# Kernel optimization log

Measured on AMD Instinct MI355X. Metric: run time of the kernel, lower is better.

Reference implementation:

```python
import jax, jax.numpy as jnp
import numpy as np

N = 50000        # n_nodes
E = 800000       # n_edges (avg degree 16)
H = 64           # hidden_size
ALPHA = 0.5      # CRF alpha
BETA = 0.5       # CRF beta
N_LAYER = 2      # args.crf_layer
GAMMA = 0.2      # LeakyReLU negative slope


def setup_inputs() -> dict:
    key = jax.random.key(0)
    k = jax.random.split(key, 5)
    emb = jax.random.normal(k[0], (N, H), jnp.float32)
    W_fc = jax.random.normal(k[1], (H, H), jnp.float32) / np.sqrt(H)
    attn_fc_w = jax.random.normal(k[2], (1, 2 * H), jnp.float32) / np.sqrt(2 * H)
    src = jax.random.randint(k[3], (E,), 0, N, dtype=jnp.int32)
    dst = jax.random.randint(k[4], (E,), 0, N, dtype=jnp.int32)
    return {"emb": emb, "W_fc": W_fc, "attn_fc_w": attn_fc_w, "src": src, "dst": dst}


def _segment_softmax(e, dst, n):
    # softmax over incoming edges of each destination node (DGL mailbox softmax)
    m = jax.ops.segment_max(e, dst, num_segments=n)
    m = jnp.where(jnp.isfinite(m), m, 0.0)  # nodes with no in-edges
    ex = jnp.exp(e - m[dst])
    denom = jax.ops.segment_sum(ex, dst, num_segments=n)
    return ex / jnp.maximum(denom[dst], 1e-16)


def reference(emb, W_fc, attn_fc_w, src, dst):
    # attn_fc(concat(z_src, z_dst)) split into two per-node projections
    a_src = attn_fc_w[0, :H]
    a_dst = attn_fc_w[0, H:]
    h = emb
    e = None
    for _ in range(N_LAYER):
        z = h @ W_fc.T                              # [N, H] emb_attn
        e = (z @ a_src)[src] + (z @ a_dst)[dst]     # [E] edge logits
        e = jnp.where(e > 0, e, GAMMA * e)          # LeakyReLU(gamma)
        att = _segment_softmax(e, dst, N)           # [E]
        crf = jax.ops.segment_sum(att[:, None] * h[src], dst, num_segments=N)  # [N, H]
        h = (ALPHA * emb + BETA * crf) / (ALPHA + BETA)
    # training loss (is_train=True); reuses last layer's edge logits e
    loss_a = jnp.sum((h - emb) ** 2, axis=-1)                     # [N]
    att = _segment_softmax(e, dst, N)
    diff = jnp.sqrt(jnp.sum((h[dst] - h[src]) ** 2, axis=-1) + 1e-12)  # [E] L2 norm
    loss_b = jax.ops.segment_sum(att * diff, dst, num_segments=N)  # [N]
    loss = jnp.mean(ALPHA * loss_a + BETA * loss_b)
    return h, loss
```

## Files before the change

### kernel.cpp

```cpp
#include <hip/hip_runtime.h>

#define NNODES 50000
#define NEDGES 800000
#define HDIM 64
#define CAP 64
#define GAMMA 0.2f
#define SCAN_B 256
#define SCAN_NB ((NNODES + SCAN_B - 1) / SCAN_B)
#define LOSS_GRID 2048
#define NPART 8
#define NODES_PER_PART ((NNODES + NPART - 1) / NPART)
#define FILL_SLICES 192
#define E4 (NEDGES / 4)
#define CHUNK ((E4 + FILL_SLICES - 1) / FILL_SLICES)

typedef unsigned short u16;
typedef unsigned int u32;

__device__ __forceinline__ u16 f2bf(float f) {
    u32 u = __float_as_uint(f);
    u32 r = (u + 0x7FFFu + ((u >> 16) & 1u)) >> 16;
    return (u16)r;
}
__device__ __forceinline__ float bflo(u32 u) { return __uint_as_float(u << 16); }
__device__ __forceinline__ float bfhi(u32 u) { return __uint_as_float(u & 0xFFFF0000u); }

__device__ __forceinline__ float wave_sum(float v) {
    #pragma unroll
    for (int off = 32; off; off >>= 1) v += __shfl_xor(v, off, 64);
    return v;
}
__device__ __forceinline__ float wave_max(float v) {
    #pragma unroll
    for (int off = 32; off; off >>= 1) v = fmaxf(v, __shfl_xor(v, off, 64));
    return v;
}
__device__ __forceinline__ int wave_sum_i(int v) {
    #pragma unroll
    for (int off = 32; off; off >>= 1) v += __shfl_xor(v, off, 64);
    return v;
}
__device__ __forceinline__ float group8_sum(float v) {
    v += __shfl_xor(v, 1, 64);
    v += __shfl_xor(v, 2, 64);
    v += __shfl_xor(v, 4, 64);
    return v;
}

__global__ __launch_bounds__(256) void k_init(int* __restrict__ cursor,
                                              float* __restrict__ lossAcc,
                                              const float* __restrict__ Wfc,
                                              const float* __restrict__ attn,
                                              float* __restrict__ ws, float* __restrict__ wd) {
    int t = threadIdx.x;
    int idx = blockIdx.x * 256 + t;
    if (idx < NNODES) cursor[idx] = 0;
    if (blockIdx.x == gridDim.x - 1) {
        if (t >= 80 && t < 96) lossAcc[t - 80] = 0.f;
        if (t >= 128) {
            int tt = t - 128;
            int k = tt & 63;
            const float* av = attn + ((tt >= 64) ? HDIM : 0);
            float s = 0.f;
            for (int j = 0; j < HDIM; ++j) s += Wfc[j * HDIM + k] * av[j];
            if (tt < 64) ws[k] = s; else wd[k] = s;
        }
    }
}

__global__ __launch_bounds__(256) void k_fillx(const int4* __restrict__ src4,
                                               const int4* __restrict__ dst4,
                                               int* __restrict__ cursor,
                                               u16* __restrict__ padded) {
    const int part = blockIdx.x & (NPART - 1);
    const int slice = blockIdx.x >> 3;
    const int lo = slice * CHUNK;
    const int hi = min(lo + CHUNK, E4);
    const int plo = part * NODES_PER_PART;
    const int phi = plo + NODES_PER_PART;
    for (int i = lo + threadIdx.x; i < hi; i += 256) {
        int4 d = dst4[i];
        bool mx = d.x >= plo && d.x < phi;
        bool my = d.y >= plo && d.y < phi;
        bool mz = d.z >= plo && d.z < phi;
        bool mw = d.w >= plo && d.w < phi;
        if (mx | my | mz | mw) {
            int4 s = src4[i];
            if (mx) { int p0 = atomicAdd(&cursor[d.x], 1); if (p0 < CAP) padded[d.x * CAP + p0] = (u16)s.x; }
            if (my) { int p1 = atomicAdd(&cursor[d.y], 1); if (p1 < CAP) padded[d.y * CAP + p1] = (u16)s.y; }
            if (mz) { int p2 = atomicAdd(&cursor[d.z], 1); if (p2 < CAP) padded[d.z * CAP + p2] = (u16)s.z; }
            if (mw) { int p3 = atomicAdd(&cursor[d.w], 1); if (p3 < CAP) padded[d.w * CAP + p3] = (u16)s.w; }
        }
    }
}

__global__ __launch_bounds__(256) void k_scan1z(const int* __restrict__ deg,
                                                int* __restrict__ blockSums,
                                                const float* __restrict__ emb,
                                                const float* __restrict__ ws,
                                                const float* __restrict__ wd,
                                                u16* __restrict__ emb_bf,
                                                float* __restrict__ zs, float* __restrict__ zd) {
    int t = threadIdx.x;
    if (blockIdx.x < SCAN_NB) {
        int idx = blockIdx.x * SCAN_B + t;
        int v = (idx < NNODES) ? min(deg[idx], CAP) : 0;
        int wsum = wave_sum_i(v);
        __shared__ int part[4];
        if ((t & 63) == 0) part[t >> 6] = wsum;
        __syncthreads();
        if (t == 0) blockSums[blockIdx.x] = part[0] + part[1] + part[2] + part[3];
    }
    int tid = blockIdx.x * blockDim.x + threadIdx.x;
    int wid = tid >> 6;
    int lane = tid & 63;
    if (wid < NNODES) {
        float v = emb[wid * HDIM + lane];
        emb_bf[wid * HDIM + lane] = f2bf(v);
        float a = wave_sum(v * ws[lane]);
        float b = wave_sum(v * wd[lane]);
        if (lane == 0) { zs[wid] = a; zd[wid] = b; }
    }
}

__global__ __launch_bounds__(SCAN_B) void k_scan3(const int* __restrict__ deg,
                                                  const int* __restrict__ blockSums,
                                                  int* __restrict__ row_ptr) {
    __shared__ int s[SCAN_B];
    int t = threadIdx.x;
    int bv = (t < SCAN_NB) ? blockSums[t] : 0;
    s[t] = bv;
    __syncthreads();
    for (int off = 1; off < SCAN_B; off <<= 1) {
        int x = (t >= off) ? s[t - off] : 0;
        __syncthreads();
        s[t] += x;
        __syncthreads();
    }
    int blockOff = (blockIdx.x > 0) ? s[blockIdx.x - 1] : 0;
    __syncthreads();
    int idx = blockIdx.x * SCAN_B + t;
    int v = (idx < NNODES) ? min(deg[idx], CAP) : 0;
    s[t] = v;
    __syncthreads();
    for (int off = 1; off < SCAN_B; off <<= 1) {
        int x = (t >= off) ? s[t - off] : 0;
        __syncthreads();
        s[t] += x;
        __syncthreads();
    }
    if (idx < NNODES) {
        int excl = s[t] - v + blockOff;
        row_ptr[idx] = excl;
        if (idx == NNODES - 1) row_ptr[NNODES] = excl + v;
    }
}

template <bool STORE_ATT, bool COMPUTE_Z, bool WRITE_F32, bool STORE_LA, bool COMPACT>
__global__ __launch_bounds__(256) void k_layer(const u16* __restrict__ hbf_in,
                                               const float* __restrict__ emb,
                                               const int* __restrict__ deg,
                                               const int* __restrict__ row_ptr,
                                               const u16* __restrict__ padded,
                                               const float* __restrict__ zs,
                                               const float* __restrict__ zd,
                                               float* __restrict__ att_csr,
                                               u16* __restrict__ csr_c,
                                               u16* __restrict__ dmap_c,
                                               float* __restrict__ h_out,
                                               u16* __restrict__ hbf_out,
                                               const float* __restrict__ ws,
                                               const float* __restrict__ wd,
                                               float* __restrict__ zs_out,
                                               float* __restrict__ zd_out,
                                               float* __restrict__ la) {
    int wid = (blockIdx.x * blockDim.x + threadIdx.x) >> 6;
    int lane = threadIdx.x & 63;
    if (wid >= NNODES) return;
    int ne = min(deg[wid], CAP);
    int s0 = 0;
    if (STORE_ATT || COMPACT) s0 = row_ptr[wid];
    float zdn = zd[wid];
    const int sub8 = lane >> 3, q8 = lane & 7;
    float acc[8];
    #pragma unroll
    for (int i = 0; i < 8; ++i) acc[i] = 0.f;

    int s = 0; float e = -INFINITY;
    bool valid = lane < ne;
    if (valid) {
        s = padded[(size_t)wid * CAP + lane];
        float z = zs[s] + zdn;
        e = z > 0.f ? z : GAMMA * z;
    }
    float m = wave_max(e);
    float ex = valid ? __expf(e - m) : 0.f;
    float dsum = wave_sum(ex);
    float inv = 1.f / fmaxf(dsum, 1e-16f);
    if (STORE_ATT && valid) att_csr[s0 + lane] = ex * inv;
    if (COMPACT && valid) {
        csr_c[s0 + lane] = (u16)s;
        dmap_c[s0 + lane] = (u16)wid;
    }
    for (int j = 0; j < ne; j += 16) {
        int ja = j + sub8, jb = j + 8 + sub8;
        float wa = __shfl(ex, ja, 64);
        float wb = __shfl(ex, jb, 64);
        int ta = __shfl(s, ja, 64);
        int tb = __shfl(s, jb, 64);
        const uint4 ra = *(const uint4*)&hbf_in[(size_t)ta * HDIM + 8 * q8];
        const uint4 rb = *(const uint4*)&hbf_in[(size_t)tb * HDIM + 8 * q8];
        acc[0] += wa * bflo(ra.x) + wb * bflo(rb.x);
        acc[1] += wa * bfhi(ra.x) + wb * bfhi(rb.x);
        acc[2] += wa * bflo(ra.y) + wb * bflo(rb.y);
        acc[3] += wa * bfhi(ra.y) + wb * bfhi(rb.y);
        acc[4] += wa * bflo(ra.z) + wb * bflo(rb.z);
        acc[5] += wa * bfhi(ra.z) + wb * bfhi(rb.z);
        acc[6] += wa * bflo(ra.w) + wb * bflo(rb.w);
        acc[7] += wa * bfhi(ra.w) + wb * bfhi(rb.w);
    }
    #pragma unroll
    for (int off = 8; off <= 32; off <<= 1) {
        #pragma unroll
        for (int i = 0; i < 8; ++i) acc[i] += __shfl_xor(acc[i], off, 64);
    }
    float hv[8];
    #pragma unroll
    for (int i = 0; i < 8; ++i) hv[i] = 0.f;
    float lap = 0.f;
    if (sub8 == 0) {
        const float4 e0 = *(const float4*)&emb[(size_t)wid * HDIM + 8 * q8];
        const float4 e1 = *(const float4*)&emb[(size_t)wid * HDIM + 8 * q8 + 4];
        hv[0] = 0.5f * (e0.x + acc[0] * inv);
        hv[1] = 0.5f * (e0.y + acc[1] * inv);
        hv[2] = 0.5f * (e0.z + acc[2] * inv);
        hv[3] = 0.5f * (e0.w + acc[3] * inv);
        hv[4] = 0.5f * (e1.x + acc[4] * inv);
        hv[5] = 0.5f * (e1.y + acc[5] * inv);
        hv[6] = 0.5f * (e1.z + acc[6] * inv);
        hv[7] = 0.5f * (e1.w + acc[7] * inv);
        if (WRITE_F32) {
            *(float4*)&h_out[(size_t)wid * HDIM + 8 * q8]     = make_float4(hv[0], hv[1], hv[2], hv[3]);
            *(float4*)&h_out[(size_t)wid * HDIM + 8 * q8 + 4] = make_float4(hv[4], hv[5], hv[6], hv[7]);
        }
        uint4 o;
        o.x = (u32)f2bf(hv[0]) | ((u32)f2bf(hv[1]) << 16);
        o.y = (u32)f2bf(hv[2]) | ((u32)f2bf(hv[3]) << 16);
        o.z = (u32)f2bf(hv[4]) | ((u32)f2bf(hv[5]) << 16);
        o.w = (u32)f2bf(hv[6]) | ((u32)f2bf(hv[7]) << 16);
        *(uint4*)&hbf_out[(size_t)wid * HDIM + 8 * q8] = o;
        if (STORE_LA) {
            float d0 = hv[0] - e0.x, d1 = hv[1] - e0.y, d2 = hv[2] - e0.z, d3 = hv[3] - e0.w;
            float d4 = hv[4] - e1.x, d5 = hv[5] - e1.y, d6 = hv[6] - e1.z, d7 = hv[7] - e1.w;
            lap = d0 * d0 + d1 * d1 + d2 * d2 + d3 * d3 +
                  d4 * d4 + d5 * d5 + d6 * d6 + d7 * d7;
        }
    }
    if (STORE_LA) {
        float lsum = wave_sum(lap);
        if (lane == 0) la[wid] = lsum;
    }
    if (COMPUTE_Z) {
        float pa = 0.f, pb = 0.f;
        if (sub8 == 0) {
            const float4 w0 = *(const float4*)&ws[8 * q8];
            const float4 w1 = *(const float4*)&ws[8 * q8 + 4];
            const float4 d0 = *(const float4*)&wd[8 * q8];
            const float4 d1 = *(const float4*)&wd[8 * q8 + 4];
            pa = hv[0] * w0.x + hv[1] * w0.y + hv[2] * w0.z + hv[3] * w0.w +
                 hv[4] * w1.x + hv[5] * w1.y + hv[6] * w1.z + hv[7] * w1.w;
            pb = hv[0] * d0.x + hv[1] * d0.y + hv[2] * d0.z + hv[3] * d0.w +
                 hv[4] * d1.x + hv[5] * d1.y + hv[6] * d1.z + hv[7] * d1.w;
        }
        float a = wave_sum(pa);
        float b = wave_sum(pb);
        if (lane == 0) { zs_out[wid] = a; zd_out[wid] = b; }
    }
}

__global__ __launch_bounds__(256) void k_loss(const float* __restrict__ la,
                                              const u16* __restrict__ hbf,
                                              const u16* __restrict__ csr_src,
                                              const u16* __restrict__ dst_map,
                                              const float* __restrict__ att_csr,
                                              float* __restrict__ acc) {
    const int lane = threadIdx.x & 63;
    const int wib = threadIdx.x >> 6;
    const int gtid = blockIdx.x * blockDim.x + threadIdx.x;
    const int nthreads = gridDim.x * blockDim.x;
    const int gw = gtid >> 6;
    const int nwaves = nthreads >> 6;
    const int sub8 = lane >> 3, q8 = lane & 7;
    float lb = 0.f;

    for (int i = gtid; i < NNODES / 4; i += nthreads) {
        const float4 v = *(const float4*)&la[i * 4];
        lb += 0.5f * (v.x + v.y + v.z + v.w);
    }
    if ((NNODES & 3) != 0 && gtid < (NNODES & 3)) lb += 0.5f * la[(NNODES & ~3) + gtid];

    for (int g = gw; g < NEDGES / 32; g += nwaves) {
        int e0 = g * 32 + sub8;
        int e1 = e0 + 8, e2 = e0 + 16, e3 = e0 + 24;
        int s0i = csr_src[e0], d0i = dst_map[e0];
        int s1i = csr_src[e1], d1i = dst_map[e1];
        int s2i = csr_src[e2], d2i = dst_map[e2];
        int s3i = csr_src[e3], d3i = dst_map[e3];
        const uint4 rs0 = *(const uint4*)&hbf[(size_t)s0i * HDIM + 8 * q8];
        const uint4 rd0 = *(const uint4*)&hbf[(size_t)d0i * HDIM + 8 * q8];
        const uint4 rs1 = *(const uint4*)&hbf[(size_t)s1i * HDIM + 8 * q8];
        const uint4 rd1 = *(const uint4*)&hbf[(size_t)d1i * HDIM + 8 * q8];
        const uint4 rs2 = *(const uint4*)&hbf[(size_t)s2i * HDIM + 8 * q8];
        const uint4 rd2 = *(const uint4*)&hbf[(size_t)d2i * HDIM + 8 * q8];
        const uint4 rs3 = *(const uint4*)&hbf[(size_t)s3i * HDIM + 8 * q8];
        const uint4 rd3 = *(const uint4*)&hbf[(size_t)d3i * HDIM + 8 * q8];
        float a0 = bflo(rd0.x) - bflo(rs0.x), a1 = bfhi(rd0.x) - bfhi(rs0.x);
        float a2 = bflo(rd0.y) - bflo(rs0.y), a3 = bfhi(rd0.y) - bfhi(rs0.y);
        float a4 = bflo(rd0.z) - bflo(rs0.z), a5 = bfhi(rd0.z) - bfhi(rs0.z);
        float a6 = bflo(rd0.w) - bflo(rs0.w), a7 = bfhi(rd0.w) - bfhi(rs0.w);
        float b0 = bflo(rd1.x) - bflo(rs1.x), b1 = bfhi(rd1.x) - bfhi(rs1.x);
        float b2 = bflo(rd1.y) - bflo(rs1.y), b3 = bfhi(rd1.y) - bfhi(rs1.y);
        float b4 = bflo(rd1.z) - bflo(rs1.z), b5 = bfhi(rd1.z) - bfhi(rs1.z);
        float b6 = bflo(rd1.w) - bflo(rs1.w), b7 = bfhi(rd1.w) - bfhi(rs1.w);
        float c0 = bflo(rd2.x) - bflo(rs2.x), c1 = bfhi(rd2.x) - bfhi(rs2.x);
        float c2 = bflo(rd2.y) - bflo(rs2.y), c3 = bfhi(rd2.y) - bfhi(rs2.y);
        float c4 = bflo(rd2.z) - bflo(rs2.z), c5 = bfhi(rd2.z) - bfhi(rs2.z);
        float c6 = bflo(rd2.w) - bflo(rs2.w), c7 = bfhi(rd2.w) - bfhi(rs2.w);
        float g0 = bflo(rd3.x) - bflo(rs3.x), g1 = bfhi(rd3.x) - bfhi(rs3.x);
        float g2 = bflo(rd3.y) - bflo(rs3.y), g3 = bfhi(rd3.y) - bfhi(rs3.y);
        float g4 = bflo(rd3.z) - bflo(rs3.z), g5 = bfhi(rd3.z) - bfhi(rs3.z);
        float g6 = bflo(rd3.w) - bflo(rs3.w), g7 = bfhi(rd3.w) - bfhi(rs3.w);
        float ss0 = group8_sum(a0 * a0 + a1 * a1 + a2 * a2 + a3 * a3 +
                               a4 * a4 + a5 * a5 + a6 * a6 + a7 * a7);
        float ss1 = group8_sum(b0 * b0 + b1 * b1 + b2 * b2 + b3 * b3 +
                               b4 * b4 + b5 * b5 + b6 * b6 + b7 * b7);
        float ss2 = group8_sum(c0 * c0 + c1 * c1 + c2 * c2 + c3 * c3 +
                               c4 * c4 + c5 * c5 + c6 * c6 + c7 * c7);
        float ss3 = group8_sum(g0 * g0 + g1 * g1 + g2 * g2 + g3 * g3 +
                               g4 * g4 + g5 * g5 + g6 * g6 + g7 * g7);
        if (q8 == 0)
            lb += 0.5f * (att_csr[e0] * sqrtf(ss0 + 1e-12f) +
                          att_csr[e1] * sqrtf(ss1 + 1e-12f) +
                          att_csr[e2] * sqrtf(ss2 + 1e-12f) +
                          att_csr[e3] * sqrtf(ss3 + 1e-12f));
    }
    lb = wave_sum(lb);
    __shared__ float part[4];
    if (lane == 0) part[wib] = lb;
    __syncthreads();
    if (threadIdx.x == 0)
        atomicAdd(acc, part[0] + part[1] + part[2] + part[3]);
}

__global__ void k_finalize(const float* __restrict__ acc, float* __restrict__ out_loss) {
    out_loss[0] = acc[0] / (float)NNODES;
}

extern "C" void kernel_launch(void* const* d_in, const int* in_sizes, int n_in,
                              void* d_out, int out_size, void* d_ws, size_t ws_size,
                              hipStream_t stream) {
    const float* emb  = (const float*)d_in[0];
    const float* Wfc  = (const float*)d_in[1];
    const float* attn = (const float*)d_in[2];
    const int*   src  = (const int*)d_in[3];
    const int*   dst  = (const int*)d_in[4];
    float* out = (float*)d_out;

    char* p = (char*)d_ws;
    int*   cursor  = (int*)p;   p += (size_t)NNODES * 4;
    float* lossAcc = (float*)p; p += 256;
    int*   row_ptr = (int*)p;   p += (size_t)(NNODES + 1) * 4;
    int*   bsums   = (int*)p;   p += (size_t)SCAN_NB * 4;
    float* wsv     = (float*)p; p += 64 * 4;
    float* wdv     = (float*)p; p += 64 * 4;
    float* zs0     = (float*)p; p += (size_t)NNODES * 4;
    float* zd0     = (float*)p; p += (size_t)NNODES * 4;
    float* zs1     = (float*)p; p += (size_t)NNODES * 4;
    float* zd1     = (float*)p; p += (size_t)NNODES * 4;
    float* laArr   = (float*)p; p += (size_t)NNODES * 4;
    float* att_csr = (float*)p; p += (size_t)NEDGES * 4;
    p = (char*)(((size_t)p + 255) & ~(size_t)255);
    u16*   padded  = (u16*)p;   p += (size_t)NNODES * CAP * 2;
    u16*   csr_src = (u16*)p;   p += (size_t)NEDGES * 2;
    u16*   dst_map = (u16*)p;   p += (size_t)NEDGES * 2;
    u16*   emb_bf  = (u16*)p;   p += (size_t)NNODES * HDIM * 2;
    u16*   h1_bf   = (u16*)p;   p += (size_t)NNODES * HDIM * 2;
    u16*   out_bf  = (u16*)p;   p += (size_t)NNODES * HDIM * 2;

    const int NB = (NNODES + 3) / 4;

    k_init<<<SCAN_NB, 256, 0, stream>>>(cursor, lossAcc, Wfc, attn, wsv, wdv);
    k_fillx<<<NPART * FILL_SLICES, 256, 0, stream>>>((const int4*)src, (const int4*)dst,
                                                     cursor, padded);
    k_scan1z<<<NB, 256, 0, stream>>>(cursor, bsums, emb, wsv, wdv, emb_bf, zs0, zd0);
    k_scan3<<<SCAN_NB, SCAN_B, 0, stream>>>(cursor, bsums, row_ptr);

    k_layer<false, true, false, false, true><<<NB, 256, 0, stream>>>(
        emb_bf, emb, cursor, row_ptr, padded, zs0, zd0,
        att_csr, csr_src, dst_map, out , h1_bf, wsv, wdv, zs1, zd1, laArr);
    k_layer<true, false, true, true, false><<<NB, 256, 0, stream>>>(
        h1_bf, emb, cursor, row_ptr, padded, zs1, zd1,
        att_csr, csr_src, dst_map, out, out_bf, wsv, wdv, zs0, zd0, laArr);

    k_loss<<<LOSS_GRID, 256, 0, stream>>>(laArr, out_bf, csr_src, dst_map, att_csr, lossAcc);
    k_finalize<<<1, 1, 0, stream>>>(lossAcc, out + (size_t)NNODES * HDIM);
}
```

Baseline: 230.1 us.

## Drop CSR compaction and recompute attention per node in loss kernel

Removes the degree scan kernels and the compacted CSR arrays (row_ptr, csr_src, dst_map, att_csr). The loss kernel now walks the padded per-node adjacency with one wave per destination node and recomputes the segment softmax from zs1/zd1. It also loads the destination row once per node instead of once per edge. This cuts two launches and the extra edge-array writes and reads, at the cost of redoing the softmax and some wasted gathers on partial 8-edge groups.

```diff
diff --git a/kernel.cpp b/kernel.cpp
--- a/kernel.cpp
+++ b/kernel.cpp
@@ -5,9 +5,8 @@
 #define HDIM 64
 #define CAP 64
 #define GAMMA 0.2f
-#define SCAN_B 256
-#define SCAN_NB ((NNODES + SCAN_B - 1) / SCAN_B)
-#define LOSS_GRID 2048
+#define INIT_B 256
+#define INIT_NB ((NNODES + INIT_B - 1) / INIT_B)
 #define NPART 8
 #define NODES_PER_PART ((NNODES + NPART - 1) / NPART)
 #define FILL_SLICES 192
@@ -33,11 +32,6 @@
 __device__ __forceinline__ float wave_max(float v) {
     #pragma unroll
     for (int off = 32; off; off >>= 1) v = fmaxf(v, __shfl_xor(v, off, 64));
-    return v;
-}
-__device__ __forceinline__ int wave_sum_i(int v) {
-    #pragma unroll
-    for (int off = 32; off; off >>= 1) v += __shfl_xor(v, off, 64);
     return v;
 }
 __device__ __forceinline__ float group8_sum(float v) {
@@ -94,23 +88,11 @@
     }
 }
 
-__global__ __launch_bounds__(256) void k_scan1z(const int* __restrict__ deg,
-                                                int* __restrict__ blockSums,
-                                                const float* __restrict__ emb,
-                                                const float* __restrict__ ws,
-                                                const float* __restrict__ wd,
-                                                u16* __restrict__ emb_bf,
-                                                float* __restrict__ zs, float* __restrict__ zd) {
-    int t = threadIdx.x;
-    if (blockIdx.x < SCAN_NB) {
-        int idx = blockIdx.x * SCAN_B + t;
-        int v = (idx < NNODES) ? min(deg[idx], CAP) : 0;
-        int wsum = wave_sum_i(v);
-        __shared__ int part[4];
-        if ((t & 63) == 0) part[t >> 6] = wsum;
-        __syncthreads();
-        if (t == 0) blockSums[blockIdx.x] = part[0] + part[1] + part[2] + part[3];
-    }
+__global__ __launch_bounds__(256) void k_zinit(const float* __restrict__ emb,
+                                               const float* __restrict__ ws,
+                                               const float* __restrict__ wd,
+                                               u16* __restrict__ emb_bf,
+                                               float* __restrict__ zs, float* __restrict__ zd) {
     int tid = blockIdx.x * blockDim.x + threadIdx.x;
     int wid = tid >> 6;
     int lane = tid & 63;
@@ -123,50 +105,13 @@
     }
 }
 
-__global__ __launch_bounds__(SCAN_B) void k_scan3(const int* __restrict__ deg,
-                                                  const int* __restrict__ blockSums,
-                                                  int* __restrict__ row_ptr) {
-    __shared__ int s[SCAN_B];
-    int t = threadIdx.x;
-    int bv = (t < SCAN_NB) ? blockSums[t] : 0;
-    s[t] = bv;
-    __syncthreads();
-    for (int off = 1; off < SCAN_B; off <<= 1) {
-        int x = (t >= off) ? s[t - off] : 0;
-        __syncthreads();
-        s[t] += x;
-        __syncthreads();
-    }
-    int blockOff = (blockIdx.x > 0) ? s[blockIdx.x - 1] : 0;
-    __syncthreads();
-    int idx = blockIdx.x * SCAN_B + t;
-    int v = (idx < NNODES) ? min(deg[idx], CAP) : 0;
-    s[t] = v;
-    __syncthreads();
-    for (int off = 1; off < SCAN_B; off <<= 1) {
-        int x = (t >= off) ? s[t - off] : 0;
-        __syncthreads();
-        s[t] += x;
-        __syncthreads();
-    }
-    if (idx < NNODES) {
-        int excl = s[t] - v + blockOff;
-        row_ptr[idx] = excl;
-        if (idx == NNODES - 1) row_ptr[NNODES] = excl + v;
-    }
-}
-
-template <bool STORE_ATT, bool COMPUTE_Z, bool WRITE_F32, bool STORE_LA, bool COMPACT>
+template <bool COMPUTE_Z, bool WRITE_F32, bool STORE_LA>
 __global__ __launch_bounds__(256) void k_layer(const u16* __restrict__ hbf_in,
                                                const float* __restrict__ emb,
                                                const int* __restrict__ deg,
-                                               const int* __restrict__ row_ptr,
                                                const u16* __restrict__ padded,
                                                const float* __restrict__ zs,
                                                const float* __restrict__ zd,
-                                               float* __restrict__ att_csr,
-                                               u16* __restrict__ csr_c,
-                                               u16* __restrict__ dmap_c,
                                                float* __restrict__ h_out,
                                                u16* __restrict__ hbf_out,
                                                const float* __restrict__ ws,
@@ -178,8 +123,6 @@
     int lane = threadIdx.x & 63;
     if (wid >= NNODES) return;
     int ne = min(deg[wid], CAP);
-    int s0 = 0;
-    if (STORE_ATT || COMPACT) s0 = row_ptr[wid];
     float zdn = zd[wid];
     const int sub8 = lane >> 3, q8 = lane & 7;
     float acc[8];
@@ -197,11 +140,6 @@
     float ex = valid ? __expf(e - m) : 0.f;
     float dsum = wave_sum(ex);
     float inv = 1.f / fmaxf(dsum, 1e-16f);
-    if (STORE_ATT && valid) att_csr[s0 + lane] = ex * inv;
-    if (COMPACT && valid) {
-        csr_c[s0 + lane] = (u16)s;
-        dmap_c[s0 + lane] = (u16)wid;
-    }
     for (int j = 0; j < ne; j += 16) {
         int ja = j + sub8, jb = j + 8 + sub8;
         float wa = __shfl(ex, ja, 64);
@@ -280,16 +218,16 @@
 
 __global__ __launch_bounds__(256) void k_loss(const float* __restrict__ la,
                                               const u16* __restrict__ hbf,
-                                              const u16* __restrict__ csr_src,
-                                              const u16* __restrict__ dst_map,
-                                              const float* __restrict__ att_csr,
+                                              const int* __restrict__ deg,
+                                              const u16* __restrict__ padded,
+                                              const float* __restrict__ zs,
+                                              const float* __restrict__ zd,
                                               float* __restrict__ acc) {
     const int lane = threadIdx.x & 63;
     const int wib = threadIdx.x >> 6;
     const int gtid = blockIdx.x * blockDim.x + threadIdx.x;
     const int nthreads = gridDim.x * blockDim.x;
-    const int gw = gtid >> 6;
-    const int nwaves = nthreads >> 6;
+    const int wid = gtid >> 6;
     const int sub8 = lane >> 3, q8 = lane & 7;
     float lb = 0.f;
 
@@ -297,59 +235,48 @@
         const float4 v = *(const float4*)&la[i * 4];
         lb += 0.5f * (v.x + v.y + v.z + v.w);
     }
-    if ((NNODES & 3) != 0 && gtid < (NNODES & 3)) lb += 0.5f * la[(NNODES & ~3) + gtid];
-
-    for (int g = gw; g < NEDGES / 32; g += nwaves) {
-        int e0 = g * 32 + sub8;
-        int e1 = e0 + 8, e2 = e0 + 16, e3 = e0 + 24;
-        int s0i = csr_src[e0], d0i = dst_map[e0];
-        int s1i = csr_src[e1], d1i = dst_map[e1];
-        int s2i = csr_src[e2], d2i = dst_map[e2];
-        int s3i = csr_src[e3], d3i = dst_map[e3];
-        const uint4 rs0 = *(const uint4*)&hbf[(size_t)s0i * HDIM + 8 * q8];
-        const uint4 rd0 = *(const uint4*)&hbf[(size_t)d0i * HDIM + 8 * q8];
-        const uint4 rs1 = *(const uint4*)&hbf[(size_t)s1i * HDIM + 8 * q8];
-        const uint4 rd1 = *(const uint4*)&hbf[(size_t)d1i * HDIM + 8 * q8];
-        const uint4 rs2 = *(const uint4*)&hbf[(size_t)s2i * HDIM + 8 * q8];
-        const uint4 rd2 = *(const uint4*)&hbf[(size_t)d2i * HDIM + 8 * q8];
-        const uint4 rs3 = *(const uint4*)&hbf[(size_t)s3i * HDIM + 8 * q8];
-        const uint4 rd3 = *(const uint4*)&hbf[(size_t)d3i * HDIM + 8 * q8];
-        float a0 = bflo(rd0.x) - bflo(rs0.x), a1 = bfhi(rd0.x) - bfhi(rs0.x);
-        float a2 = bflo(rd0.y) - bflo(rs0.y), a3 = bfhi(rd0.y) - bfhi(rs0.y);
-        float a4 = bflo(rd0.z) - bflo(rs0.z), a5 = bfhi(rd0.z) - bfhi(rs0.z);
-        float a6 = bflo(rd0.w) - bflo(rs0.w), a7 = bfhi(rd0.w) - bfhi(rs0.w);
-        float b0 = bflo(rd1.x) - bflo(rs1.x), b1 = bfhi(rd1.x) - bfhi(rs1.x);
-        float b2 = bflo(rd1.y) - bflo(rs1.y), b3 = bfhi(rd1.y) - bfhi(rs1.y);
-        float b4 = bflo(rd1.z) - bflo(rs1.z), b5 = bfhi(rd1.z) - bfhi(rs1.z);
-        float b6 = bflo(rd1.w) - bflo(rs1.w), b7 = bfhi(rd1.w) - bfhi(rs1.w);
-        float c0 = bflo(rd2.x) - bflo(rs2.x), c1 = bfhi(rd2.x) - bfhi(rs2.x);
-        float c2 = bflo(rd2.y) - bflo(rs2.y), c3 = bfhi(rd2.y) - bfhi(rs2.y);
-        float c4 = bflo(rd2.z) - bflo(rs2.z), c5 = bfhi(rd2.z) - bfhi(rs2.z);
-        float c6 = bflo(rd2.w) - bflo(rs2.w), c7 = bfhi(rd2.w) - bfhi(rs2.w);
-        float g0 = bflo(rd3.x) - bflo(rs3.x), g1 = bfhi(rd3.x) - bfhi(rs3.x);
-        float g2 = bflo(rd3.y) - bflo(rs3.y), g3 = bfhi(rd3.y) - bfhi(rs3.y);
-        float g4 = bflo(rd3.z) - bflo(rs3.z), g5 = bfhi(rd3.z) - bfhi(rs3.z);
-        float g6 = bflo(rd3.w) - bflo(rs3.w), g7 = bfhi(rd3.w) - bfhi(rs3.w);
-        float ss0 = group8_sum(a0 * a0 + a1 * a1 + a2 * a2 + a3 * a3 +
-                               a4 * a4 + a5 * a5 + a6 * a6 + a7 * a7);
-        float ss1 = group8_sum(b0 * b0 + b1 * b1 + b2 * b2 + b3 * b3 +
-                               b4 * b4 + b5 * b5 + b6 * b6 + b7 * b7);
-        float ss2 = group8_sum(c0 * c0 + c1 * c1 + c2 * c2 + c3 * c3 +
-                               c4 * c4 + c5 * c5 + c6 * c6 + c7 * c7);
-        float ss3 = group8_sum(g0 * g0 + g1 * g1 + g2 * g2 + g3 * g3 +
-                               g4 * g4 + g5 * g5 + g6 * g6 + g7 * g7);
-        if (q8 == 0)
-            lb += 0.5f * (att_csr[e0] * sqrtf(ss0 + 1e-12f) +
-                          att_csr[e1] * sqrtf(ss1 + 1e-12f) +
-                          att_csr[e2] * sqrtf(ss2 + 1e-12f) +
-                          att_csr[e3] * sqrtf(ss3 + 1e-12f));
+
+    if (wid < NNODES) {
+        int ne = min(deg[wid], CAP);
+        if (ne > 0) {
+            float zdn = zd[wid];
+            int s = 0; float e = -INFINITY;
+            bool valid = lane < ne;
+            if (valid) {
+                s = padded[(size_t)wid * CAP + lane];
+                float z = zs[s] + zdn;
+                e = z > 0.f ? z : GAMMA * z;
+            }
+            float m = wave_max(e);
+            float ex = valid ? __expf(e - m) : 0.f;
+            float dsum = wave_sum(ex);
+            float att = ex * (1.f / fmaxf(dsum, 1e-16f));
+            const uint4 rd = *(const uint4*)&hbf[(size_t)wid * HDIM + 8 * q8];
+            const float h0 = bflo(rd.x), h1 = bfhi(rd.x), h2 = bflo(rd.y), h3 = bfhi(rd.y);
+            const float h4 = bflo(rd.z), h5 = bfhi(rd.z), h6 = bflo(rd.w), h7 = bfhi(rd.w);
+            float part = 0.f;
+            for (int j = 0; j < ne; j += 8) {
+                int jj = j + sub8;
+                float w = __shfl(att, jj, 64);
+                int t = __shfl(s, jj, 64);
+                const uint4 r = *(const uint4*)&hbf[(size_t)t * HDIM + 8 * q8];
+                float d0 = bflo(r.x) - h0, d1 = bfhi(r.x) - h1;
+                float d2 = bflo(r.y) - h2, d3 = bfhi(r.y) - h3;
+                float d4 = bflo(r.z) - h4, d5 = bfhi(r.z) - h5;
+                float d6 = bflo(r.w) - h6, d7 = bfhi(r.w) - h7;
+                float ss = group8_sum(d0 * d0 + d1 * d1 + d2 * d2 + d3 * d3 +
+                                      d4 * d4 + d5 * d5 + d6 * d6 + d7 * d7);
+                if (q8 == 0) part += w * sqrtf(ss + 1e-12f);
+            }
+            lb += 0.5f * part;
+        }
     }
     lb = wave_sum(lb);
-    __shared__ float part[4];
-    if (lane == 0) part[wib] = lb;
+    __shared__ float psum[4];
+    if (lane == 0) psum[wib] = lb;
     __syncthreads();
     if (threadIdx.x == 0)
-        atomicAdd(acc, part[0] + part[1] + part[2] + part[3]);
+        atomicAdd(acc, psum[0] + psum[1] + psum[2] + psum[3]);
 }
 
 __global__ void k_finalize(const float* __restrict__ acc, float* __restrict__ out_loss) {
@@ -369,8 +296,6 @@
     char* p = (char*)d_ws;
     int*   cursor  = (int*)p;   p += (size_t)NNODES * 4;
     float* lossAcc = (float*)p; p += 256;
-    int*   row_ptr = (int*)p;   p += (size_t)(NNODES + 1) * 4;
-    int*   bsums   = (int*)p;   p += (size_t)SCAN_NB * 4;
     float* wsv     = (float*)p; p += 64 * 4;
     float* wdv     = (float*)p; p += 64 * 4;
     float* zs0     = (float*)p; p += (size_t)NNODES * 4;
@@ -378,30 +303,26 @@
     float* zs1     = (float*)p; p += (size_t)NNODES * 4;
     float* zd1     = (float*)p; p += (size_t)NNODES * 4;
     float* laArr   = (float*)p; p += (size_t)NNODES * 4;
-    float* att_csr = (float*)p; p += (size_t)NEDGES * 4;
     p = (char*)(((size_t)p + 255) & ~(size_t)255);
     u16*   padded  = (u16*)p;   p += (size_t)NNODES * CAP * 2;
-    u16*   csr_src = (u16*)p;   p += (size_t)NEDGES * 2;
-    u16*   dst_map = (u16*)p;   p += (size_t)NEDGES * 2;
     u16*   emb_bf  = (u16*)p;   p += (size_t)NNODES * HDIM * 2;
     u16*   h1_bf   = (u16*)p;   p += (size_t)NNODES * HDIM * 2;
     u16*   out_bf  = (u16*)p;   p += (size_t)NNODES * HDIM * 2;
 
     const int NB = (NNODES + 3) / 4;
 
-    k_init<<<SCAN_NB, 256, 0, stream>>>(cursor, lossAcc, Wfc, attn, wsv, wdv);
+    k_init<<<INIT_NB, 256, 0, stream>>>(cursor, lossAcc, Wfc, attn, wsv, wdv);
     k_fillx<<<NPART * FILL_SLICES, 256, 0, stream>>>((const int4*)src, (const int4*)dst,
                                                      cursor, padded);
-    k_scan1z<<<NB, 256, 0, stream>>>(cursor, bsums, emb, wsv, wdv, emb_bf, zs0, zd0);
-    k_scan3<<<SCAN_NB, SCAN_B, 0, stream>>>(cursor, bsums, row_ptr);
-
-    k_layer<false, true, false, false, true><<<NB, 256, 0, stream>>>(
-        emb_bf, emb, cursor, row_ptr, padded, zs0, zd0,
-        att_csr, csr_src, dst_map, out , h1_bf, wsv, wdv, zs1, zd1, laArr);
-    k_layer<true, false, true, true, false><<<NB, 256, 0, stream>>>(
-        h1_bf, emb, cursor, row_ptr, padded, zs1, zd1,
-        att_csr, csr_src, dst_map, out, out_bf, wsv, wdv, zs0, zd0, laArr);
-
-    k_loss<<<LOSS_GRID, 256, 0, stream>>>(laArr, out_bf, csr_src, dst_map, att_csr, lossAcc);
+    k_zinit<<<NB, 256, 0, stream>>>(emb, wsv, wdv, emb_bf, zs0, zd0);
+
+    k_layer<true, false, false><<<NB, 256, 0, stream>>>(
+        emb_bf, emb, cursor, padded, zs0, zd0,
+        out , h1_bf, wsv, wdv, zs1, zd1, laArr);
+    k_layer<false, true, true><<<NB, 256, 0, stream>>>(
+        h1_bf, emb, cursor, padded, zs1, zd1,
+        out, out_bf, wsv, wdv, zs0, zd0, laArr);
+
+    k_loss<<<NB, 256, 0, stream>>>(laArr, out_bf, cursor, padded, zs1, zd1, lossAcc);
     k_finalize<<<1, 1, 0, stream>>>(lossAcc, out + (size_t)NNODES * HDIM);
 }
```

After: 351.8 us. 1.53x slower.
